# Kernel tuning notes

Hardware: AMD Instinct MI355X
Metric: run time of the kernel (lower is better)

## Reference

```python
import jax, jax.numpy as jnp
import numpy as np

HEAD_SIZE = 128
D_MODEL = 1024


def setup_inputs() -> dict:
    key = jax.random.key(0)
    kx, kq, kk, kv = jax.random.split(key, 4)
    B, T, C = 8, 2048, D_MODEL
    scale = 1.0 / np.sqrt(C)
    x = jax.random.normal(kx, (B, T, C), dtype=jnp.float32)
    # Dense(head_size, use_bias=False) weights, shape [C, head_size]
    Wq = jax.random.normal(kq, (C, HEAD_SIZE), dtype=jnp.float32) * scale
    Wk = jax.random.normal(kk, (C, HEAD_SIZE), dtype=jnp.float32) * scale
    Wv = jax.random.normal(kv, (C, HEAD_SIZE), dtype=jnp.float32) * scale
    return {"x": x, "Wq": Wq, "Wk": Wk, "Wv": Wv}


def reference(x, Wq, Wk, Wv):
    B, T, C = x.shape
    q = jnp.einsum('btc,ch->bth', x, Wq)  # [B,T,H]
    k = jnp.einsum('btc,ch->bth', x, Wk)
    v = jnp.einsum('btc,ch->bth', x, Wv)
    # NOTE: original scales by C**-0.5 (input channels), not head_size**-0.5
    scale = jnp.asarray(C, x.dtype) ** -0.5
    wei = jnp.einsum('bqh,bkh->bqk', q, k) * scale  # [B,T,T]
    causal = jnp.tril(jnp.ones((T, T), dtype=bool))
    wei = jnp.where(causal, wei, -jnp.inf)
    wei = jax.nn.softmax(wei, axis=-1)
    # dropout is identity in inference mode
    out = jnp.einsum('bqk,bkh->bqh', wei, v)  # [B,T,H]
    return out
```

## Files before the change

### kernel.cpp

```cpp
#include <hip/hip_runtime.h>

#define HS 128
#define DM 1024
#define BB 8
#define TT 2048

typedef __bf16 bf16;
typedef __bf16 bf16x8 __attribute__((ext_vector_type(8)));
typedef float f32x4 __attribute__((ext_vector_type(4)));

#define MFMA16(a, b, c) __builtin_amdgcn_mfma_f32_16x16x32_bf16(a, b, c, 0, 0, 0)
#define RAW_BARRIER() asm volatile("s_barrier" ::: "memory")

__device__ __forceinline__ void gll16(const bf16* g, bf16* l) {
  __builtin_amdgcn_global_load_lds(
      (const __attribute__((address_space(1))) void*)g,
      (__attribute__((address_space(3))) void*)l, 16, 0, 0);
}
__device__ __forceinline__ void gll16f(const float* g, float* l) {
  __builtin_amdgcn_global_load_lds(
      (const __attribute__((address_space(1))) void*)g,
      (__attribute__((address_space(3))) void*)l, 16, 0, 0);
}

__global__ __launch_bounds__(256) void wt_kernel(const float* __restrict__ Wq,
                                                 const float* __restrict__ Wk,
                                                 const float* __restrict__ Wv,
                                                 bf16* __restrict__ Wt) {
  __shared__ bf16 lt[128][72];
  const int mat = blockIdx.y;
  const float* W = mat == 0 ? Wq : (mat == 1 ? Wk : Wv);
  const int k0 = blockIdx.x * 64;
  const int t = threadIdx.x;
  for (int i = 0; i < 32; ++i) {
    int idx = t + i * 256;
    int k = idx >> 7;
    int h = idx & 127;
    lt[h][k] = (bf16)W[(size_t)(k0 + k) * HS + h];
  }
  __syncthreads();
  int h = t >> 1, half = t & 1;
  const uint4* src = (const uint4*)&lt[h][half * 32];
  uint4* dst = (uint4*)(Wt + ((size_t)mat * 128 + h) * DM + k0 + half * 32);
  dst[0] = src[0]; dst[1] = src[1]; dst[2] = src[2]; dst[3] = src[3];
}

__global__ __launch_bounds__(256) void qkv_kernel(const float* __restrict__ x,
                                                  const bf16* __restrict__ Wt,
                                                  bf16* __restrict__ Q,
                                                  bf16* __restrict__ K,
                                                  bf16* __restrict__ V) {
  __shared__ __align__(16) float xsf[2][4096];
  __shared__ __align__(16) bf16 wsb[2][12288];
  const int t = threadIdx.x, w = t >> 6, lane = t & 63, rl = lane & 15, quad = lane >> 4;
  const int rt = blockIdx.x >> 1, nb = blockIdx.x & 1;
  const int row0 = rt * 64;
  const int rw = w & 1, cw = w >> 1;
  f32x4 acc[2][6] = {};

  auto stage = [&](int kt, int bufi) {
#pragma unroll
    for (int i2 = 0; i2 < 4; ++i2) {
      int s = w * 4 + i2;
      int row = s * 4 + (lane >> 4);
      int cg = (lane & 15) ^ (row & 15);
      gll16f(x + (size_t)(row0 + row) * DM + kt * 64 + cg * 4, &xsf[bufi][s * 256]);
    }
#pragma unroll
    for (int i2 = 0; i2 < 6; ++i2) {
      int s = w * 6 + i2;
      int row = s * 8 + (lane >> 3);
      int cg = (lane & 7) ^ (row & 7);
      gll16(Wt + (size_t)(nb * 192 + row) * DM + kt * 64 + cg * 8, &wsb[bufi][s * 512]);
    }
  };

  stage(0, 0);
  stage(1, 1);
  for (int kt = 0; kt < 16; ++kt) {
    const int cur = kt & 1;
    if (kt < 15) asm volatile("s_waitcnt vmcnt(10)" ::: "memory");
    else         asm volatile("s_waitcnt vmcnt(0)" ::: "memory");
    RAW_BARRIER();
#pragma unroll
    for (int kc = 0; kc < 2; ++kc) {
      bf16x8 a[2];
#pragma unroll
      for (int rf = 0; rf < 2; ++rf) {
        int ar = rw * 32 + rf * 16 + rl;
        int c0 = kc * 8 + quad * 2;
        float4 f0 = *(const float4*)&xsf[cur][ar * 64 + (((c0) ^ (ar & 15)) << 2)];
        float4 f1 = *(const float4*)&xsf[cur][ar * 64 + (((c0 + 1) ^ (ar & 15)) << 2)];
        bf16x8 tv;
        tv[0] = (bf16)f0.x; tv[1] = (bf16)f0.y; tv[2] = (bf16)f0.z; tv[3] = (bf16)f0.w;
        tv[4] = (bf16)f1.x; tv[5] = (bf16)f1.y; tv[6] = (bf16)f1.z; tv[7] = (bf16)f1.w;
        a[rf] = tv;
      }
#pragma unroll
      for (int cf = 0; cf < 6; ++cf) {
        int br = cw * 96 + cf * 16 + rl;
        int cb = kc * 4 + quad;
        bf16x8 bb = *(const bf16x8*)&wsb[cur][br * 64 + ((cb ^ (br & 7)) << 3)];
        acc[0][cf] = MFMA16(a[0], bb, acc[0][cf]);
        acc[1][cf] = MFMA16(a[1], bb, acc[1][cf]);
      }
    }
    RAW_BARRIER();
    if (kt < 14) stage(kt + 2, cur);
  }
#pragma unroll
  for (int cf = 0; cf < 6; ++cf) {
    int cg = nb * 192 + cw * 96 + cf * 16 + rl;
    int mat = cg >> 7, hcol = cg & 127;
    bf16* dst = mat == 0 ? Q : (mat == 1 ? K : V);
#pragma unroll
    for (int rf = 0; rf < 2; ++rf)
#pragma unroll
      for (int r = 0; r < 4; ++r) {
        int tg = row0 + rw * 32 + rf * 16 + quad * 4 + r;
        dst[((size_t)tg << 7) + hcol] = (bf16)acc[rf][cf][r];
      }
  }
}

__global__ __launch_bounds__(256) void vtrans(const bf16* __restrict__ V,
                                              bf16* __restrict__ Vt) {
  __shared__ __align__(16) bf16 lt[4096];
  const int t = threadIdx.x;
  const int tt = blockIdx.x >> 1, hb = blockIdx.x & 1;
  const int t0 = tt * 64, h0 = hb * 64;
  const int r = t >> 2, seg = t & 3;
  bf16x8 a = *(const bf16x8*)(V + (size_t)(t0 + r) * HS + h0 + seg * 16);
  bf16x8 b2 = *(const bf16x8*)(V + (size_t)(t0 + r) * HS + h0 + seg * 16 + 8);
#pragma unroll
  for (int e = 0; e < 8; ++e) {
    int h = seg * 16 + e;
    lt[h * 64 + (((r >> 3) ^ (h & 7)) << 3) + (r & 7)] = a[e];
  }
#pragma unroll
  for (int e = 0; e < 8; ++e) {
    int h = seg * 16 + 8 + e;
    lt[h * 64 + (((r >> 3) ^ (h & 7)) << 3) + (r & 7)] = b2[e];
  }
  __syncthreads();
  const int hr = t >> 2, sg = t & 3;
  bf16x8 o0 = *(const bf16x8*)(lt + hr * 64 + (((sg * 2) ^ (hr & 7)) << 3));
  bf16x8 o1 = *(const bf16x8*)(lt + hr * 64 + (((sg * 2 + 1) ^ (hr & 7)) << 3));
  const int bidx = t0 >> 11, tt0 = t0 & 2047;
  bf16* dst = Vt + ((size_t)(bidx * 128 + h0 + hr) << 11) + tt0 + sg * 16;
  *(bf16x8*)dst = o0;
  *(bf16x8*)(dst + 8) = o1;
}

__global__ __launch_bounds__(256) void attn_kernel(const bf16* __restrict__ Qb,
                                                   const bf16* __restrict__ Kb,
                                                   const bf16* __restrict__ Vtb,
                                                   float* __restrict__ out) {
  __shared__ __align__(16) char smem[79104];
  bf16* qs = (bf16*)smem;
  bf16* ks = (bf16*)(smem + 8192);
  bf16* vt = (bf16*)(smem + 40960);
  float* Of = (float*)smem;
  float* ml = (float*)(smem + 78848);
  const int t = threadIdx.x, w = t >> 6, lane = t & 63, rl = lane & 15, quad = lane >> 4;
  const int wrow = w >> 1, kh = w & 1;
  const int rank = blockIdx.x >> 3, b = blockIdx.x & 7;
  const int qi = 63 - rank;
  const int q0 = qi * 32;
  const size_t base = (size_t)b * TT;
  const int KT = (qi >> 1) + 1;

#pragma unroll
  for (int i2 = 0; i2 < 2; ++i2) {
    int s = w * 2 + i2;
    int row = s * 4 + (lane >> 4);
    int ch = (lane & 15) ^ (row & 15);
    gll16(Qb + ((base + q0 + row) << 7) + ch * 8, qs + s * 512);
  }
  auto stageKV = [&](int slot) {
    int kt = min(slot, KT - 1);
    int bufi = slot & 1;
    bf16* ksb = ks + bufi * 8192;
    bf16* vtb = vt + bufi * 8192;
#pragma unroll
    for (int i2 = 0; i2 < 4; ++i2) {
      int s = w * 4 + i2;
      int rowk = s * 4 + (lane >> 4);
      int chk = (lane & 15) ^ (rowk & 15);
      gll16(Kb + ((base + kt * 64 + rowk) << 7) + chk * 8, ksb + s * 512);
      int rowv = s * 8 + (lane >> 3);
      int chv = (lane & 7) ^ (rowv & 7);
      gll16(Vtb + ((size_t)(b * 128 + rowv) << 11) + kt * 64 + chv * 8, vtb + s * 512);
    }
  };
  stageKV(0);
  stageKV(1);

  f32x4 o[8] = {};
  float lrow[4] = {0.f, 0.f, 0.f, 0.f};
  bf16* psw = (bf16*)(smem + 73728) + w * 640;

  for (int i = 0; i < KT; ++i) {
    const int cur = i & 1;
    asm volatile("s_waitcnt vmcnt(8)" ::: "memory");
    RAW_BARRIER();
    bf16* ksb = ks + cur * 8192;
    bf16* vtb = vt + cur * 8192;
    f32x4 s4[2] = {};
#pragma unroll
    for (int hc = 0; hc < 4; ++hc) {
      int arow = wrow * 16 + rl;
      bf16x8 a = *(const bf16x8*)(qs + arow * 128 + ((((hc << 2) + quad) ^ (arow & 15)) << 3));
#pragma unroll
      for (int c = 0; c < 2; ++c) {
        int brow = (kh * 2 + c) * 16 + rl;
        bf16x8 bb = *(const bf16x8*)(ksb + brow * 128 + ((((hc << 2) + quad) ^ (brow & 15)) << 3));
        s4[c] = MFMA16(a, bb, s4[c]);
      }
    }
    const bool diag = (i == KT - 1);
#pragma unroll
    for (int r = 0; r < 4; ++r) {
      int rloc = quad * 4 + r;
      int rowg = q0 + wrow * 16 + rloc;
      float psum = 0.f;
#pragma unroll
      for (int c = 0; c < 2; ++c) {
        int colg = i * 64 + kh * 32 + c * 16 + rl;
        float p = (diag && colg > rowg) ? 0.f : __expf(s4[c][r] * 0.03125f - 6.0f);
        psum += p;
        psw[rloc * 40 + c * 16 + rl] = (bf16)p;
      }
      lrow[r] += psum;
    }
    bf16x8 pa = *(const bf16x8*)(psw + rl * 40 + quad * 8);
#pragma unroll
    for (int ht = 0; ht < 8; ++ht) {
      int brow = ht * 16 + rl;
      bf16x8 bb = *(const bf16x8*)(vtb + brow * 64 + ((((kh << 2) + quad) ^ (brow & 7)) << 3));
      o[ht] = MFMA16(pa, bb, o[ht]);
    }
    RAW_BARRIER();
    if (i + 2 <= KT) stageKV(i + 2);
  }

#pragma unroll
  for (int r = 0; r < 4; ++r)
#pragma unroll
    for (int off = 1; off < 16; off <<= 1) lrow[r] += __shfl_xor(lrow[r], off, 64);
  __syncthreads();
#pragma unroll
  for (int ht = 0; ht < 8; ++ht)
#pragma unroll
    for (int r = 0; r < 4; ++r)
      Of[kh * 4096 + (wrow * 16 + quad * 4 + r) * 128 + ht * 16 + rl] = o[ht][r];
  if (rl == 0)
#pragma unroll
    for (int r = 0; r < 4; ++r) ml[kh * 32 + wrow * 16 + quad * 4 + r] = lrow[r];
  __syncthreads();
#pragma unroll
  for (int r = 0; r < 4; ++r) {
    int rowl = wrow * 16 + quad * 4 + r;
    float inv = 1.f / (ml[rowl] + ml[32 + rowl]);
#pragma unroll
    for (int hh = 0; hh < 4; ++hh) {
      int col = kh * 64 + hh * 16 + rl;
      out[((base + q0 + rowl) << 7) + col] =
          (Of[rowl * 128 + col] + Of[4096 + rowl * 128 + col]) * inv;
    }
  }
}

extern "C" void kernel_launch(void* const* d_in, const int* in_sizes, int n_in,
                              void* d_out, int out_size, void* d_ws, size_t ws_size,
                              hipStream_t stream) {
  const float* x = (const float*)d_in[0];
  const float* Wq = (const float*)d_in[1];
  const float* Wk = (const float*)d_in[2];
  const float* Wv = (const float*)d_in[3];
  float* out = (float*)d_out;
  char* ws = (char*)d_ws;
  bf16* Wt = (bf16*)ws;
  bf16* Q = (bf16*)(ws + 786432);
  bf16* K = (bf16*)(ws + 786432 + 4194304);
  bf16* V = (bf16*)(ws + 786432 + 2 * 4194304);
  bf16* Vt = (bf16*)(ws + 786432 + 3 * 4194304);
  wt_kernel<<<dim3(16, 3), 256, 0, stream>>>(Wq, Wk, Wv, Wt);
  qkv_kernel<<<dim3(512), 256, 0, stream>>>(x, Wt, Q, K, V);
  vtrans<<<dim3(512), 256, 0, stream>>>(V, Vt);
  attn_kernel<<<dim3(512), 256, 0, stream>>>(Q, K, Vt, out);
}
```

Baseline: 154.0 us.

## Fuse V transpose into QKV projection epilogue and hoist Q fragments

The QKV projection now writes V directly in transposed layout: the V tile is staged through shared memory and written out as Vt with vector stores. This removes the separate vtrans kernel launch and the intermediate V round trip through global memory. In the attention kernel, the Q operand fragments are loaded from LDS once into registers instead of on every key tile, which adds register pressure. The shared V staging area reuses the x/W buffers after the main loop, and the __syncthreads sits inside an nb==1 branch; this is safe only because that condition is uniform per block.

```diff
diff --git a/kernel.cpp b/kernel.cpp
--- a/kernel.cpp
+++ b/kernel.cpp
@@ -49,9 +49,11 @@
                                                   const bf16* __restrict__ Wt,
                                                   bf16* __restrict__ Q,
                                                   bf16* __restrict__ K,
-                                                  bf16* __restrict__ V) {
-  __shared__ __align__(16) float xsf[2][4096];
-  __shared__ __align__(16) bf16 wsb[2][12288];
+                                                  bf16* __restrict__ Vt) {
+  __shared__ __align__(16) char qsm[81920];
+  float (*xsf)[4096] = (float(*)[4096])qsm;
+  bf16 (*wsb)[12288] = (bf16(*)[12288])(qsm + 32768);
+  bf16* vts = (bf16*)qsm;
   const int t = threadIdx.x, w = t >> 6, lane = t & 63, rl = lane & 15, quad = lane >> 4;
   const int rt = blockIdx.x >> 1, nb = blockIdx.x & 1;
   const int row0 = rt * 64;
@@ -112,44 +114,34 @@
   for (int cf = 0; cf < 6; ++cf) {
     int cg = nb * 192 + cw * 96 + cf * 16 + rl;
     int mat = cg >> 7, hcol = cg & 127;
-    bf16* dst = mat == 0 ? Q : (mat == 1 ? K : V);
-#pragma unroll
-    for (int rf = 0; rf < 2; ++rf)
-#pragma unroll
-      for (int r = 0; r < 4; ++r) {
-        int tg = row0 + rw * 32 + rf * 16 + quad * 4 + r;
-        dst[((size_t)tg << 7) + hcol] = (bf16)acc[rf][cf][r];
-      }
-  }
-}
-
-__global__ __launch_bounds__(256) void vtrans(const bf16* __restrict__ V,
-                                              bf16* __restrict__ Vt) {
-  __shared__ __align__(16) bf16 lt[4096];
-  const int t = threadIdx.x;
-  const int tt = blockIdx.x >> 1, hb = blockIdx.x & 1;
-  const int t0 = tt * 64, h0 = hb * 64;
-  const int r = t >> 2, seg = t & 3;
-  bf16x8 a = *(const bf16x8*)(V + (size_t)(t0 + r) * HS + h0 + seg * 16);
-  bf16x8 b2 = *(const bf16x8*)(V + (size_t)(t0 + r) * HS + h0 + seg * 16 + 8);
-#pragma unroll
-  for (int e = 0; e < 8; ++e) {
-    int h = seg * 16 + e;
-    lt[h * 64 + (((r >> 3) ^ (h & 7)) << 3) + (r & 7)] = a[e];
-  }
-#pragma unroll
-  for (int e = 0; e < 8; ++e) {
-    int h = seg * 16 + 8 + e;
-    lt[h * 64 + (((r >> 3) ^ (h & 7)) << 3) + (r & 7)] = b2[e];
-  }
-  __syncthreads();
-  const int hr = t >> 2, sg = t & 3;
-  bf16x8 o0 = *(const bf16x8*)(lt + hr * 64 + (((sg * 2) ^ (hr & 7)) << 3));
-  bf16x8 o1 = *(const bf16x8*)(lt + hr * 64 + (((sg * 2 + 1) ^ (hr & 7)) << 3));
-  const int bidx = t0 >> 11, tt0 = t0 & 2047;
-  bf16* dst = Vt + ((size_t)(bidx * 128 + h0 + hr) << 11) + tt0 + sg * 16;
-  *(bf16x8*)dst = o0;
-  *(bf16x8*)(dst + 8) = o1;
+    if (mat < 2) {
+      bf16* dst = mat == 0 ? Q : K;
+#pragma unroll
+      for (int rf = 0; rf < 2; ++rf)
+#pragma unroll
+        for (int r = 0; r < 4; ++r) {
+          int tg = row0 + rw * 32 + rf * 16 + quad * 4 + r;
+          dst[((size_t)tg << 7) + hcol] = (bf16)acc[rf][cf][r];
+        }
+    } else {
+#pragma unroll
+      for (int rf = 0; rf < 2; ++rf)
+#pragma unroll
+        for (int r = 0; r < 4; ++r) {
+          int trow = rw * 32 + rf * 16 + quad * 4 + r;
+          vts[hcol * 72 + trow] = (bf16)acc[rf][cf][r];
+        }
+    }
+  }
+  if (nb == 1) {
+    __syncthreads();
+    const int h = t >> 1, half = t & 1;
+    const bf16* src = vts + h * 72 + half * 32;
+    bf16* dst = Vt + ((size_t)((row0 >> 11) * 128 + h) << 11) + (row0 & 2047) + half * 32;
+#pragma unroll
+    for (int j = 0; j < 4; ++j)
+      ((bf16x8*)dst)[j] = ((const bf16x8*)src)[j];
+  }
 }
 
 __global__ __launch_bounds__(256) void attn_kernel(const bf16* __restrict__ Qb,
@@ -198,24 +190,29 @@
 
   f32x4 o[8] = {};
   float lrow[4] = {0.f, 0.f, 0.f, 0.f};
+  bf16x8 aq[4];
   bf16* psw = (bf16*)(smem + 73728) + w * 640;
 
   for (int i = 0; i < KT; ++i) {
     const int cur = i & 1;
     asm volatile("s_waitcnt vmcnt(8)" ::: "memory");
     RAW_BARRIER();
+    if (i == 0) {
+      const int arow = wrow * 16 + rl;
+#pragma unroll
+      for (int hc = 0; hc < 4; ++hc)
+        aq[hc] = *(const bf16x8*)(qs + arow * 128 + ((((hc << 2) + quad) ^ (arow & 15)) << 3));
+    }
     bf16* ksb = ks + cur * 8192;
     bf16* vtb = vt + cur * 8192;
     f32x4 s4[2] = {};
 #pragma unroll
     for (int hc = 0; hc < 4; ++hc) {
-      int arow = wrow * 16 + rl;
-      bf16x8 a = *(const bf16x8*)(qs + arow * 128 + ((((hc << 2) + quad) ^ (arow & 15)) << 3));
 #pragma unroll
       for (int c = 0; c < 2; ++c) {
         int brow = (kh * 2 + c) * 16 + rl;
         bf16x8 bb = *(const bf16x8*)(ksb + brow * 128 + ((((hc << 2) + quad) ^ (brow & 15)) << 3));
-        s4[c] = MFMA16(a, bb, s4[c]);
+        s4[c] = MFMA16(aq[hc], bb, s4[c]);
       }
     }
     const bool diag = (i == KT - 1);
@@ -283,10 +280,8 @@
   bf16* Wt = (bf16*)ws;
   bf16* Q = (bf16*)(ws + 786432);
   bf16* K = (bf16*)(ws + 786432 + 4194304);
-  bf16* V = (bf16*)(ws + 786432 + 2 * 4194304);
-  bf16* Vt = (bf16*)(ws + 786432 + 3 * 4194304);
+  bf16* Vt = (bf16*)(ws + 786432 + 2 * 4194304);
   wt_kernel<<<dim3(16, 3), 256, 0, stream>>>(Wq, Wk, Wv, Wt);
-  qkv_kernel<<<dim3(512), 256, 0, stream>>>(x, Wt, Q, K, V);
-  vtrans<<<dim3(512), 256, 0, stream>>>(V, Vt);
+  qkv_kernel<<<dim3(512), 256, 0, stream>>>(x, Wt, Q, K, Vt);
   attn_kernel<<<dim3(512), 256, 0, stream>>>(Q, K, Vt, out);
 }
```

Measured after the change: 152.8 us. Within noise of the previous version (-0.8%).
